# Kernel optimization log

Measured on AMD Instinct MI355X. Metric: run time of the kernel, lower is better.

## Reference

```python
import jax, jax.numpy as jnp
import numpy as np

IN_FEATURES = 1024
OUT_FEATURES = 1024
DEGREE = 8
BATCH = 8192


def setup_inputs() -> dict:
    key = jax.random.key(0)
    kx, kc = jax.random.split(key)
    x = jax.random.normal(kx, (BATCH, IN_FEATURES), dtype=jnp.float32)
    std = 1.0 / (IN_FEATURES * (DEGREE + 1))
    coefficients = std * jax.random.normal(
        kc, (IN_FEATURES, OUT_FEATURES, DEGREE + 1), dtype=jnp.float32)
    return {"x": x, "coefficients": coefficients}


def reference(x, coefficients):
    # x: (B, I); coefficients: (I, O, D+1)
    t = jnp.tanh(x)
    # Chebyshev recursion T_0=1, T_1=t, T_k = 2 t T_{k-1} - T_{k-2}
    vals = [jnp.ones_like(t), t]
    for _ in range(2, DEGREE + 1):
        vals.append(2.0 * t * vals[-1] - vals[-2])
    cheby = jnp.stack(vals, axis=-1)  # (B, I, D+1)
    return jnp.einsum('bid,iod->bo', cheby, coefficients)
```

## Files before the change

kernel.cpp:

```cpp
#include <hip/hip_runtime.h>
#include <hip/hip_bf16.h>
#include <stdint.h>

#define BATCH 8192
#define INF   1024
#define GN    1024
#define GK    8192

typedef __attribute__((ext_vector_type(4))) float floatx4;
typedef __attribute__((ext_vector_type(8))) short short8;

static __device__ __forceinline__ ushort f2bf(float f) {
  union { float f; uint32_t u; } v; v.f = f;
  uint32_t r = v.u + 0x7FFF + ((v.u >> 16) & 1);
  return (ushort)(r >> 16);
}

__global__ void bias_kernel(const float* __restrict__ coef, float* __restrict__ bias) {
  const int o = threadIdx.x;
  const int i0 = blockIdx.x << 5;
  float s = 0.f;
  #pragma unroll
  for (int ii = 0; ii < 32; ++ii)
    s += coef[(size_t)(i0 + ii) * 9216 + (size_t)o * 9];
  atomicAdd(&bias[o], s);
}

__global__ __launch_bounds__(256) void repack(const float* __restrict__ coef,
                                              ushort* __restrict__ Wt) {
  __shared__ ushort lds[32 * 9 * 33];
  const int i0 = (blockIdx.x >> 5) << 5;
  const int o0 = (blockIdx.x & 31) << 5;
  const int t = threadIdx.x;
  for (int idx = t; idx < 32 * 288; idx += 256) {
    const int ii  = idx / 288;
    const int rem = idx - ii * 288;
    const float f = coef[(size_t)(i0 + ii) * 9216 + (size_t)o0 * 9 + rem];
    lds[rem * 33 + ii] = f2bf(f);
  }
  __syncthreads();
  for (int idx = t; idx < 32 * 8 * 32; idx += 256) {
    const int oo  = idx >> 8;
    const int rem = idx & 255;
    const int d1  = rem >> 5;
    const int ii  = rem & 31;
    Wt[(size_t)(o0 + oo) * GK + (size_t)d1 * 1024 + (i0 + ii)] =
        lds[(oo * 9 + d1 + 1) * 33 + ii];
  }
}

__global__ __launch_bounds__(256) void featurize(const float* __restrict__ x,
                                                 ushort* __restrict__ Cf) {
  const int tid = blockIdx.x * 256 + threadIdx.x;
  const size_t idx4 = (size_t)tid << 2;
  const int b = tid >> 8;
  const int i = (tid & 255) << 2;
  const float4 v = *reinterpret_cast<const float4*>(x + idx4);
  float t[4] = {tanhf(v.x), tanhf(v.y), tanhf(v.z), tanhf(v.w)};
  float Tp[4] = {1.f, 1.f, 1.f, 1.f};
  float Tc[4] = {t[0], t[1], t[2], t[3]};
  ushort* base = Cf + (size_t)b * GK + i;
  #pragma unroll
  for (int d = 1; d <= 8; ++d) {
    ushort4 u;
    u.x = f2bf(Tc[0]); u.y = f2bf(Tc[1]); u.z = f2bf(Tc[2]); u.w = f2bf(Tc[3]);
    *reinterpret_cast<ushort4*>(base + (size_t)(d - 1) * 1024) = u;
    #pragma unroll
    for (int j = 0; j < 4; ++j) {
      const float Tn = 2.f * t[j] * Tc[j] - Tp[j];
      Tp[j] = Tc[j]; Tc[j] = Tn;
    }
  }
}

__global__ __launch_bounds__(256) void gemm_bt(const ushort* __restrict__ A,
                                               const ushort* __restrict__ Bt,
                                               const float* __restrict__ bias,
                                               float* __restrict__ C) {
  __shared__ __align__(16) ushort As[128 * 32];
  __shared__ __align__(16) ushort Bs[128 * 32];
  const int t = threadIdx.x;
  const int bid = (blockIdx.x & 7) * 64 + (blockIdx.x >> 3);
  const int bm0 = (bid >> 3) << 7;
  const int bn0 = (bid & 7) << 7;
  const int lane = t & 63;
  const int wid = t >> 6;
  const int wm0 = (wid >> 1) << 6;
  const int wn0 = (wid & 1) << 6;
  const int lr = lane & 15;
  const int lk = lane >> 4;

  const int srow  = t >> 2;
  const int scolb = (t & 3) << 4;

  const char* gA0 = (const char*)(A  + (size_t)(bm0 + srow) * GK) + scolb;
  const char* gB0 = (const char*)(Bt + (size_t)(bn0 + srow) * GK) + scolb;
  const size_t rstride = (size_t)64 * GK * 2;

  floatx4 acc[4][4] = {};

  for (int k0 = 0; k0 < GK; k0 += 32) {
    const size_t kb = (size_t)k0 * 2;
    __builtin_amdgcn_global_load_lds(
        (const __attribute__((address_space(1))) void*)(gA0 + kb),
        (__attribute__((address_space(3))) void*)((char*)As + t * 16), 16, 0, 0);
    __builtin_amdgcn_global_load_lds(
        (const __attribute__((address_space(1))) void*)(gA0 + kb + rstride),
        (__attribute__((address_space(3))) void*)((char*)As + 4096 + t * 16), 16, 0, 0);
    __builtin_amdgcn_global_load_lds(
        (const __attribute__((address_space(1))) void*)(gB0 + kb),
        (__attribute__((address_space(3))) void*)((char*)Bs + t * 16), 16, 0, 0);
    __builtin_amdgcn_global_load_lds(
        (const __attribute__((address_space(1))) void*)(gB0 + kb + rstride),
        (__attribute__((address_space(3))) void*)((char*)Bs + 4096 + t * 16), 16, 0, 0);
    __syncthreads();

    short8 af[4], bf[4];
    #pragma unroll
    for (int mi = 0; mi < 4; ++mi)
      af[mi] = *reinterpret_cast<const short8*>(&As[(wm0 + mi * 16 + lr) * 32 + lk * 8]);
    #pragma unroll
    for (int ni = 0; ni < 4; ++ni)
      bf[ni] = *reinterpret_cast<const short8*>(&Bs[(wn0 + ni * 16 + lr) * 32 + lk * 8]);
    #pragma unroll
    for (int mi = 0; mi < 4; ++mi)
      #pragma unroll
      for (int ni = 0; ni < 4; ++ni)
        acc[mi][ni] = __builtin_amdgcn_mfma_f32_16x16x32_bf16(af[mi], bf[ni], acc[mi][ni], 0, 0, 0);
    __syncthreads();
  }

  #pragma unroll
  for (int ni = 0; ni < 4; ++ni) {
    const int col = bn0 + wn0 + ni * 16 + lr;
    const float bv = bias[col];
    #pragma unroll
    for (int mi = 0; mi < 4; ++mi) {
      const int row = bm0 + wm0 + mi * 16 + lk * 4;
      #pragma unroll
      for (int r = 0; r < 4; ++r)
        C[(size_t)(row + r) * GN + col] = acc[mi][ni][r] + bv;
    }
  }
}

extern "C" void kernel_launch(void* const* d_in, const int* in_sizes, int n_in,
                              void* d_out, int out_size, void* d_ws, size_t ws_size,
                              hipStream_t stream) {
  const float* x    = (const float*)d_in[0];
  const float* coef = (const float*)d_in[1];
  float* out = (float*)d_out;

  char* ws = (char*)d_ws;
  ushort* Cf   = (ushort*)ws;
  ushort* Wt   = (ushort*)(ws + (size_t)BATCH * GK * 2);
  float*  bias = (float*)(ws + (size_t)BATCH * GK * 2 + (size_t)GN * GK * 2);

  hipMemsetAsync(bias, 0, GN * sizeof(float), stream);
  bias_kernel<<<32, 1024, 0, stream>>>(coef, bias);
  repack<<<1024, 256, 0, stream>>>(coef, Wt);
  featurize<<<(BATCH * INF / 4) / 256, 256, 0, stream>>>(x, Cf);
  gemm_bt<<<512, 256, 0, stream>>>(Cf, Wt, bias, out);
}
```

Measured before the change: 310.3 us.

## Double-buffer GEMM LDS tiles with BK=64 and XOR swizzle; fuse bias into repack

The GEMM now stages 64-wide K tiles into two LDS buffers. The next tile's global-to-LDS loads are issued before computing on the current one, and the barriers per tile drop from two to one. Rows are XOR-swizzled in LDS to avoid bank conflicts on the 128-byte row stride. The separate bias-reduction kernel is folded into the repack kernel, removing one launch and a strided re-read of the coefficients. The cost is four times the LDS per block (64KB), which may reduce occupancy.

```diff
diff --git a/kernel.cpp b/kernel.cpp
--- a/kernel.cpp
+++ b/kernel.cpp
@@ -16,19 +16,11 @@
   return (ushort)(r >> 16);
 }
 
-__global__ void bias_kernel(const float* __restrict__ coef, float* __restrict__ bias) {
-  const int o = threadIdx.x;
-  const int i0 = blockIdx.x << 5;
-  float s = 0.f;
-  #pragma unroll
-  for (int ii = 0; ii < 32; ++ii)
-    s += coef[(size_t)(i0 + ii) * 9216 + (size_t)o * 9];
-  atomicAdd(&bias[o], s);
-}
-
 __global__ __launch_bounds__(256) void repack(const float* __restrict__ coef,
-                                              ushort* __restrict__ Wt) {
+                                              ushort* __restrict__ Wt,
+                                              float* __restrict__ bias) {
   __shared__ ushort lds[32 * 9 * 33];
+  __shared__ float  bl[32 * 33];
   const int i0 = (blockIdx.x >> 5) << 5;
   const int o0 = (blockIdx.x & 31) << 5;
   const int t = threadIdx.x;
@@ -37,8 +29,16 @@
     const int rem = idx - ii * 288;
     const float f = coef[(size_t)(i0 + ii) * 9216 + (size_t)o0 * 9 + rem];
     lds[rem * 33 + ii] = f2bf(f);
+    const int oo = rem / 9;
+    if (rem == oo * 9) bl[oo * 33 + ii] = f;
   }
   __syncthreads();
+  if (t < 32) {
+    float s = 0.f;
+    #pragma unroll
+    for (int ii = 0; ii < 32; ++ii) s += bl[t * 33 + ii];
+    atomicAdd(&bias[o0 + t], s);
+  }
   for (int idx = t; idx < 32 * 8 * 32; idx += 256) {
     const int oo  = idx >> 8;
     const int rem = idx & 255;
@@ -77,8 +77,8 @@
                                                const ushort* __restrict__ Bt,
                                                const float* __restrict__ bias,
                                                float* __restrict__ C) {
-  __shared__ __align__(16) ushort As[128 * 32];
-  __shared__ __align__(16) ushort Bs[128 * 32];
+  __shared__ __align__(16) ushort As[2][128 * 64];
+  __shared__ __align__(16) ushort Bs[2][128 * 64];
   const int t = threadIdx.x;
   const int bid = (blockIdx.x & 7) * 64 + (blockIdx.x >> 3);
   const int bm0 = (bid >> 3) << 7;
@@ -90,45 +90,67 @@
   const int lr = lane & 15;
   const int lk = lane >> 4;
 
-  const int srow  = t >> 2;
-  const int scolb = (t & 3) << 4;
+  const int srow = t >> 3;
+  const int scol = (((t & 7) ^ (srow & 7)) << 4);
+  const char* gA0 = (const char*)(A  + (size_t)(bm0 + srow) * GK) + scol;
+  const char* gB0 = (const char*)(Bt + (size_t)(bn0 + srow) * GK) + scol;
+  const size_t rstride = (size_t)32 * GK * 2;
 
-  const char* gA0 = (const char*)(A  + (size_t)(bm0 + srow) * GK) + scolb;
-  const char* gB0 = (const char*)(Bt + (size_t)(bn0 + srow) * GK) + scolb;
-  const size_t rstride = (size_t)64 * GK * 2;
+  const int rc0 = ((0 + lk) ^ (lr & 7)) << 4;
+  const int rc1 = ((4 + lk) ^ (lr & 7)) << 4;
 
   floatx4 acc[4][4] = {};
 
-  for (int k0 = 0; k0 < GK; k0 += 32) {
-    const size_t kb = (size_t)k0 * 2;
-    __builtin_amdgcn_global_load_lds(
-        (const __attribute__((address_space(1))) void*)(gA0 + kb),
-        (__attribute__((address_space(3))) void*)((char*)As + t * 16), 16, 0, 0);
-    __builtin_amdgcn_global_load_lds(
-        (const __attribute__((address_space(1))) void*)(gA0 + kb + rstride),
-        (__attribute__((address_space(3))) void*)((char*)As + 4096 + t * 16), 16, 0, 0);
-    __builtin_amdgcn_global_load_lds(
-        (const __attribute__((address_space(1))) void*)(gB0 + kb),
-        (__attribute__((address_space(3))) void*)((char*)Bs + t * 16), 16, 0, 0);
-    __builtin_amdgcn_global_load_lds(
-        (const __attribute__((address_space(1))) void*)(gB0 + kb + rstride),
-        (__attribute__((address_space(3))) void*)((char*)Bs + 4096 + t * 16), 16, 0, 0);
+#define STAGE(bufi, k0)                                                        \
+  do {                                                                         \
+    const size_t kb = (size_t)(k0) * 2;                                        \
+    _Pragma("unroll")                                                          \
+    for (int j = 0; j < 4; ++j) {                                              \
+      __builtin_amdgcn_global_load_lds(                                        \
+          (const __attribute__((address_space(1))) void*)(gA0 + kb + j * rstride), \
+          (__attribute__((address_space(3))) void*)((char*)As[bufi] + j * 4096 + t * 16), \
+          16, 0, 0);                                                           \
+      __builtin_amdgcn_global_load_lds(                                        \
+          (const __attribute__((address_space(1))) void*)(gB0 + kb + j * rstride), \
+          (__attribute__((address_space(3))) void*)((char*)Bs[bufi] + j * 4096 + t * 16), \
+          16, 0, 0);                                                           \
+    }                                                                          \
+  } while (0)
+
+  STAGE(0, 0);
+  __syncthreads();
+
+  int cur = 0;
+  for (int kt = 0; kt < GK / 64; ++kt) {
+    if (kt < GK / 64 - 1) {
+      if (cur) STAGE(0, (kt + 1) * 64); else STAGE(1, (kt + 1) * 64);
+    }
+    const char* Ab = (const char*)As[cur];
+    const char* Bb = (const char*)Bs[cur];
+    short8 af[4][2], bf[4][2];
+    #pragma unroll
+    for (int mi = 0; mi < 4; ++mi) {
+      const int rb = (wm0 + mi * 16 + lr) * 128;
+      af[mi][0] = *reinterpret_cast<const short8*>(Ab + rb + rc0);
+      af[mi][1] = *reinterpret_cast<const short8*>(Ab + rb + rc1);
+    }
+    #pragma unroll
+    for (int ni = 0; ni < 4; ++ni) {
+      const int rb = (wn0 + ni * 16 + lr) * 128;
+      bf[ni][0] = *reinterpret_cast<const short8*>(Bb + rb + rc0);
+      bf[ni][1] = *reinterpret_cast<const short8*>(Bb + rb + rc1);
+    }
+    #pragma unroll
+    for (int kk = 0; kk < 2; ++kk)
+      #pragma unroll
+      for (int mi = 0; mi < 4; ++mi)
+        #pragma unroll
+        for (int ni = 0; ni < 4; ++ni)
+          acc[mi][ni] = __builtin_amdgcn_mfma_f32_16x16x32_bf16(af[mi][kk], bf[ni][kk], acc[mi][ni], 0, 0, 0);
     __syncthreads();
-
-    short8 af[4], bf[4];
-    #pragma unroll
-    for (int mi = 0; mi < 4; ++mi)
-      af[mi] = *reinterpret_cast<const short8*>(&As[(wm0 + mi * 16 + lr) * 32 + lk * 8]);
-    #pragma unroll
-    for (int ni = 0; ni < 4; ++ni)
-      bf[ni] = *reinterpret_cast<const short8*>(&Bs[(wn0 + ni * 16 + lr) * 32 + lk * 8]);
-    #pragma unroll
-    for (int mi = 0; mi < 4; ++mi)
-      #pragma unroll
-      for (int ni = 0; ni < 4; ++ni)
-        acc[mi][ni] = __builtin_amdgcn_mfma_f32_16x16x32_bf16(af[mi], bf[ni], acc[mi][ni], 0, 0, 0);
-    __syncthreads();
+    cur ^= 1;
   }
+#undef STAGE
 
   #pragma unroll
   for (int ni = 0; ni < 4; ++ni) {
@@ -157,8 +179,7 @@
   float*  bias = (float*)(ws + (size_t)BATCH * GK * 2 + (size_t)GN * GK * 2);
 
   hipMemsetAsync(bias, 0, GN * sizeof(float), stream);
-  bias_kernel<<<32, 1024, 0, stream>>>(coef, bias);
-  repack<<<1024, 256, 0, stream>>>(coef, Wt);
+  repack<<<1024, 256, 0, stream>>>(coef, Wt, bias);
   featurize<<<(BATCH * INF / 4) / 256, 256, 0, stream>>>(x, Cf);
   gemm_bt<<<512, 256, 0, stream>>>(Cf, Wt, bias, out);
 }
```

Measured after the change: 274.7 us. -11.5%, faster.
